# Optimization experiments

Measured on AMD Instinct MI355X. Metric: run time of the kernel, lower is better.

## Reference

```python
import jax, jax.numpy as jnp
import numpy as np

STATE_DIM = 5
HIDDEN = 32
B, S = 128, 4096
D_IN = STATE_DIM + 1 + 3  # [h_prev, temp_seq, direction]


def setup_inputs() -> dict:
    key = jax.random.key(0)
    ks = jax.random.split(key, 16)
    g = lambda k, shp: (jax.random.normal(k, shp, dtype=jnp.float32) * 0.1)
    z = lambda shp: jnp.zeros(shp, jnp.float32)
    inp = {}
    inp["h_prev"] = jax.random.normal(ks[0], (B, S, STATE_DIM), dtype=jnp.float32)
    inp["delta_x"] = jax.random.uniform(ks[1], (B, S, 6), dtype=jnp.float32)
    # internal layer 0 (input D_IN -> HIDDEN), layer 1 (HIDDEN -> HIDDEN)
    inp["Wa0"] = g(ks[2], (D_IN, HIDDEN)); inp["ba0"] = z((HIDDEN,))
    inp["Wb0"] = g(ks[3], (D_IN, HIDDEN)); inp["bb0"] = z((HIDDEN,))
    inp["Wa1"] = g(ks[4], (HIDDEN, HIDDEN)); inp["ba1"] = z((HIDDEN,))
    inp["Wb1"] = g(ks[5], (HIDDEN, HIDDEN)); inp["bb1"] = z((HIDDEN,))
    inp["W_alpha"] = g(ks[6], (HIDDEN, 1)); inp["b_alpha"] = z((1,))
    inp["W_beta"]  = g(ks[7], (HIDDEN, 1)); inp["b_beta"]  = z((1,))
    inp["W_gamma"] = g(ks[8], (HIDDEN, 1)); inp["b_gamma"] = z((1,))
    inp["W_c"] = g(ks[9], (HIDDEN, STATE_DIM)); inp["b_c"] = z((STATE_DIM,))
    inp["W_out"] = g(ks[10], (STATE_DIM, 1))  # no bias
    return inp


def reference(h_prev, delta_x, Wa0, ba0, Wb0, bb0, Wa1, ba1, Wb1, bb1,
              W_alpha, b_alpha, W_beta, b_beta, W_gamma, b_gamma,
              W_c, b_c, W_out):
    # delta_x: [delta_strain, delta_time, delta_temp, init_strain, init_time, init_temp]
    df = delta_x[..., :3]                       # (B, S, 3)
    init_temp = delta_x[:, 0:1, 5:6]            # (B, 1, 1) init temp at t=0
    temp_seq = jnp.cumsum(delta_x[..., 2:3], axis=1) + init_temp  # (B, S, 1)
    # normalized increment direction
    norm = jnp.maximum(jnp.sqrt(jnp.sum(df * df, axis=-1, keepdims=True)), 1e-7)
    direction = df / norm                       # (B, S, 3)
    l = jnp.concatenate([h_prev, temp_seq, direction], axis=-1)   # (B, S, 9)
    # two internal tanh*tanh gated dense layers
    l = jnp.tanh(l @ Wa0 + ba0) * jnp.tanh(l @ Wb0 + bb0)         # (B, S, 32)
    l = jnp.tanh(l @ Wa1 + ba1) * jnp.tanh(l @ Wb1 + bb1)         # (B, S, 32)
    # exp gates (non-negative rate params)
    alpha = jnp.exp(l @ W_alpha + b_alpha)      # (B, S, 1)
    beta  = jnp.exp(l @ W_beta  + b_beta)
    gamma = jnp.exp(l @ W_gamma + b_gamma)
    c_n = jnp.tanh(l @ W_c + b_c)               # (B, S, 5)
    # update gate from physical increments
    z = 1.0 - jnp.exp(-alpha * jnp.abs(df[..., 0:1])
                      - beta * df[..., 1:2]
                      - gamma * jnp.abs(df[..., 2:3]))
    h_n = (1.0 - z) * h_prev + z * c_n          # (B, S, 5)
    sigma_n = h_n @ W_out                       # (B, S, 1)
    return (h_n, sigma_n)
```

## Files before the change

kernel.cpp:

```cpp
#include <hip/hip_runtime.h>

#define B_DIMC   128
#define S_DIMC   4096
#define N_TOK    (B_DIMC * S_DIMC)
#define CHUNK    256
#define N_CHUNK  (N_TOK / CHUNK)
#define CPB      (S_DIMC / CHUNK)

typedef __attribute__((ext_vector_type(8))) short  short8;
typedef __attribute__((ext_vector_type(4))) float  floatx4;
typedef __attribute__((ext_vector_type(4))) int    intx4;

__device__ __forceinline__ int cvtpk(float a, float b) {
    int r;
    asm("v_cvt_pk_bf16_f32 %0, %1, %2" : "=v"(r) : "v"(a), "v"(b));
    return r;
}
__device__ __forceinline__ short bf1(float a) { return (short)cvtpk(a, a); }

__device__ __forceinline__ float fast_tanh(float x) {
    float e = __builtin_amdgcn_exp2f(2.885390082f * __builtin_amdgcn_fmed3f(x, -9.0f, 9.0f));
    return fmaf(-2.0f, __builtin_amdgcn_rcpf(e + 1.0f), 1.0f);
}
__device__ __forceinline__ float gate2(float a, float b) {
    const float c = 2.885390082f;
    float ea = __builtin_amdgcn_exp2f(c * __builtin_amdgcn_fmed3f(a, -9.0f, 9.0f));
    float eb = __builtin_amdgcn_exp2f(c * __builtin_amdgcn_fmed3f(b, -9.0f, 9.0f));
    float t  = fmaf(ea, eb, 1.0f);
    float u  = ea + eb;
    return (t - u) * __builtin_amdgcn_rcpf(t + u);
}

__device__ __forceinline__ float head_w(int n, int k,
                                        const float* Wal, const float* Wbe,
                                        const float* Wga, const float* Wc) {
    if (n == 0) return Wal[k];
    if (n == 1) return Wbe[k];
    if (n == 2) return Wga[k];
    if (n < 8)  return Wc[k * 5 + (n - 3)];
    return 0.0f;
}

union SMemU {
    struct {
        short W[4][32][40];
        short Wh[16][40];
        float Bias[16];
        float Wsum[4];
        float Wpre[4];
    } b;
    short A[4][64][40];
};

__global__ __launch_bounds__(256) void msc_kernel(
    const float* __restrict__ h_prev, const float* __restrict__ dx,
    const float* __restrict__ Wa0, const float* __restrict__ ba0,
    const float* __restrict__ Wb0, const float* __restrict__ bb0,
    const float* __restrict__ Wa1, const float* __restrict__ ba1,
    const float* __restrict__ Wb1, const float* __restrict__ bb1,
    const float* __restrict__ W_alpha, const float* __restrict__ b_alpha,
    const float* __restrict__ W_beta,  const float* __restrict__ b_beta,
    const float* __restrict__ W_gamma, const float* __restrict__ b_gamma,
    const float* __restrict__ W_c,     const float* __restrict__ b_c,
    const float* __restrict__ W_out,
    float* __restrict__ out)
{
    __shared__ __align__(16) SMemU sm;

    const int tid  = threadIdx.x;
    const int w    = tid >> 6;
    const int lane = tid & 63;
    const int n    = lane & 15;
    const int quad = lane >> 4;
    const int t    = blockIdx.x * CHUNK + tid;

    const float* hp = h_prev + (size_t)t * 5;
    const float* d  = dx     + (size_t)t * 6;
    const float hp0 = hp[0], hp1 = hp[1], hp2 = hp[2], hp3 = hp[3], hp4 = hp[4];
    const float df0 = d[0], df1 = d[1], df2 = d[2];

    const int batch = blockIdx.x / CPB;
    const int cib   = blockIdx.x % CPB;
    const float* dxb = dx + (size_t)batch * S_DIMC * 6;
    const int npre = cib * CHUNK;
    float ps = 0.0f;
    for (int s = tid; s < npre; s += 256)
        ps += dxb[(size_t)s * 6 + 2];
    ps += __shfl_xor(ps, 1, 64);
    ps += __shfl_xor(ps, 2, 64);
    ps += __shfl_xor(ps, 4, 64);
    ps += __shfl_xor(ps, 8, 64);
    ps += __shfl_xor(ps, 16, 64);
    ps += __shfl_xor(ps, 32, 64);
    if (lane == 0) sm.b.Wpre[w] = ps;

    float w5a[2], w5b[2], bA0[2], bB0[2], bA1[2], bB1[2];
    #pragma unroll
    for (int nt = 0; nt < 2; ++nt) {
        const int col = nt * 16 + n;
        w5a[nt] = Wa0[5 * 32 + col];  w5b[nt] = Wb0[5 * 32 + col];
        bA0[nt] = ba0[col];           bB0[nt] = bb0[col];
        bA1[nt] = ba1[col];           bB1[nt] = bb1[col];
    }

    float x = df2;
    #pragma unroll
    for (int off = 1; off < 64; off <<= 1) {
        float y = __shfl_up(x, off, 64);
        if (lane >= off) x += y;
    }
    if (lane == 63) sm.b.Wsum[w] = x;

    #pragma unroll
    for (int m = 0; m < 4; ++m) {
        const float* Wsrc = (m == 0) ? Wa0 : (m == 1) ? Wb0 : (m == 2) ? Wa1 : Wb1;
        const bool l0 = (m < 2);
        #pragma unroll
        for (int dd = tid; dd < 512; dd += 256) {
            const int col = dd >> 4, kd = dd & 15, k0 = kd * 2, k1 = k0 + 1;
            float v0, v1;
            if (l0) {
                v0 = (k0 < 9 && k0 != 5) ? Wsrc[k0 * 32 + col] : 0.0f;
                v1 = (k1 < 9 && k1 != 5) ? Wsrc[k1 * 32 + col] : 0.0f;
            } else {
                v0 = Wsrc[k0 * 32 + col];
                v1 = Wsrc[k1 * 32 + col];
            }
            ((int*)&sm.b.W[m][col][0])[kd] = cvtpk(v0, v1);
        }
    }
    {
        const int hn = tid >> 4, kd = tid & 15, k0 = kd * 2;
        const float v0 = head_w(hn, k0,     W_alpha, W_beta, W_gamma, W_c);
        const float v1 = head_w(hn, k0 + 1, W_alpha, W_beta, W_gamma, W_c);
        ((int*)&sm.b.Wh[hn][0])[kd] = cvtpk(v0, v1);
    }
    if (tid < 16) {
        sm.b.Bias[tid] = (tid == 0) ? b_alpha[0] : (tid == 1) ? b_beta[0]
                       : (tid == 2) ? b_gamma[0] : (tid < 8) ? b_c[tid - 3] : 0.0f;
    }

    __syncthreads();

    short8 Ba0f[2], Bb0f[2], Ba1f[2], Bb1f[2], Bhf;
    #pragma unroll
    for (int nt = 0; nt < 2; ++nt) {
        const int col = nt * 16 + n;
        Ba0f[nt] = *(const short8*)&sm.b.W[0][col][quad * 8];
        Bb0f[nt] = *(const short8*)&sm.b.W[1][col][quad * 8];
        Ba1f[nt] = *(const short8*)&sm.b.W[2][col][quad * 8];
        Bb1f[nt] = *(const short8*)&sm.b.W[3][col][quad * 8];
    }
    Bhf = *(const short8*)&sm.b.Wh[n][quad * 8];
    const float hbias = sm.b.Bias[n];

    const float coff = dxb[5]
        + (sm.b.Wpre[0] + sm.b.Wpre[1] + sm.b.Wpre[2] + sm.b.Wpre[3]);
    float pre = coff;
    if (w > 0) pre += sm.b.Wsum[0];
    if (w > 1) pre += sm.b.Wsum[1];
    if (w > 2) pre += sm.b.Wsum[2];
    const float temp_t = pre + x;

    __syncthreads();

    const float nrm = fmaxf(sqrtf(df0*df0 + df1*df1 + df2*df2), 1e-7f);
    const float inv = __builtin_amdgcn_rcpf(nrm);
    {
        int* arow = (int*)&sm.A[w][lane][0];
        intx4 v0 = { cvtpk(hp0, hp1), cvtpk(hp2, hp3),
                     cvtpk(hp4, 0.0f), cvtpk(df0*inv, df1*inv) };
        intx4 v1 = { cvtpk(df2*inv, 0.0f), 0, 0, 0 };
        intx4 z4 = { 0, 0, 0, 0 };
        *(intx4*)&arow[0]  = v0;
        *(intx4*)&arow[4]  = v1;
        *(intx4*)&arow[8]  = z4;
        *(intx4*)&arow[12] = z4;
        *(float*)&arow[16] = temp_t;
    }

    #pragma unroll
    for (int mt = 0; mt < 4; ++mt) {
        const short8 Af = *(const short8*)&sm.A[w][mt * 16 + n][quad * 8];
        const int rb = mt * 16 + quad * 4;
        floatx4 tv;
        #pragma unroll
        for (int r = 0; r < 4; ++r)
            tv[r] = *(const float*)&sm.A[w][rb + r][32];
        #pragma unroll
        for (int nt = 0; nt < 2; ++nt) {
            floatx4 Ca, Cb;
            #pragma unroll
            for (int r = 0; r < 4; ++r) {
                Ca[r] = fmaf(tv[r], w5a[nt], bA0[nt]);
                Cb[r] = fmaf(tv[r], w5b[nt], bB0[nt]);
            }
            Ca = __builtin_amdgcn_mfma_f32_16x16x32_bf16(Af, Ba0f[nt], Ca, 0, 0, 0);
            Cb = __builtin_amdgcn_mfma_f32_16x16x32_bf16(Af, Bb0f[nt], Cb, 0, 0, 0);
            #pragma unroll
            for (int r = 0; r < 4; ++r)
                sm.A[w][mt * 16 + quad * 4 + r][nt * 16 + n] = bf1(gate2(Ca[r], Cb[r]));
        }
    }

    #pragma unroll
    for (int mt = 0; mt < 4; ++mt) {
        const short8 Af = *(const short8*)&sm.A[w][mt * 16 + n][quad * 8];
        #pragma unroll
        for (int nt = 0; nt < 2; ++nt) {
            floatx4 Ca = { bA1[nt], bA1[nt], bA1[nt], bA1[nt] };
            floatx4 Cb = { bB1[nt], bB1[nt], bB1[nt], bB1[nt] };
            Ca = __builtin_amdgcn_mfma_f32_16x16x32_bf16(Af, Ba1f[nt], Ca, 0, 0, 0);
            Cb = __builtin_amdgcn_mfma_f32_16x16x32_bf16(Af, Bb1f[nt], Cb, 0, 0, 0);
            #pragma unroll
            for (int r = 0; r < 4; ++r)
                sm.A[w][mt * 16 + quad * 4 + r][nt * 16 + n] = bf1(gate2(Ca[r], Cb[r]));
        }
    }

    short8 Ah[4];
    #pragma unroll
    for (int mt = 0; mt < 4; ++mt)
        Ah[mt] = *(const short8*)&sm.A[w][mt * 16 + n][quad * 8];
    asm volatile("" ::: "memory");

    float* hc = (float*)&sm.A[w][0][0];
    #pragma unroll
    for (int mt = 0; mt < 4; ++mt) {
        floatx4 C = { hbias, hbias, hbias, hbias };
        C = __builtin_amdgcn_mfma_f32_16x16x32_bf16(Ah[mt], Bhf, C, 0, 0, 0);
        if (n < 8) {
            #pragma unroll
            for (int r = 0; r < 4; ++r)
                hc[(mt * 16 + quad * 4 + r) * 12 + n] = C[r];
        }
    }
    asm volatile("" ::: "memory");

    const floatx4 h0v = *(const floatx4*)&hc[lane * 12];
    const floatx4 h1v = *(const floatx4*)&hc[lane * 12 + 4];

    const float alpha = __expf(h0v[0]);
    const float beta  = __expf(h0v[1]);
    const float gamma = __expf(h0v[2]);
    const float z     = 1.0f - __expf(-(alpha * fabsf(df0) + beta * df1 + gamma * fabsf(df2)));
    const float omz   = 1.0f - z;

    const float c0 = fast_tanh(h0v[3]), c1 = fast_tanh(h1v[0]), c2 = fast_tanh(h1v[1]),
                c3 = fast_tanh(h1v[2]), c4 = fast_tanh(h1v[3]);

    const float hn0 = omz * hp0 + z * c0;
    const float hn1 = omz * hp1 + z * c1;
    const float hn2 = omz * hp2 + z * c2;
    const float hn3 = omz * hp3 + z * c3;
    const float hn4 = omz * hp4 + z * c4;

    float* out_h = out + (size_t)t * 5;
    out_h[0] = hn0; out_h[1] = hn1; out_h[2] = hn2; out_h[3] = hn3; out_h[4] = hn4;
    out[(size_t)N_TOK * 5 + t] =
        hn0 * W_out[0] + hn1 * W_out[1] + hn2 * W_out[2] + hn3 * W_out[3] + hn4 * W_out[4];
}

extern "C" void kernel_launch(void* const* d_in, const int* in_sizes, int n_in,
                              void* d_out, int out_size, void* d_ws, size_t ws_size,
                              hipStream_t stream) {
    const float* h_prev  = (const float*)d_in[0];
    const float* dx      = (const float*)d_in[1];
    const float* Wa0     = (const float*)d_in[2];
    const float* ba0     = (const float*)d_in[3];
    const float* Wb0     = (const float*)d_in[4];
    const float* bb0     = (const float*)d_in[5];
    const float* Wa1     = (const float*)d_in[6];
    const float* ba1     = (const float*)d_in[7];
    const float* Wb1     = (const float*)d_in[8];
    const float* bb1     = (const float*)d_in[9];
    const float* W_alpha = (const float*)d_in[10];
    const float* b_alpha = (const float*)d_in[11];
    const float* W_beta  = (const float*)d_in[12];
    const float* b_beta  = (const float*)d_in[13];
    const float* W_gamma = (const float*)d_in[14];
    const float* b_gamma = (const float*)d_in[15];
    const float* W_c     = (const float*)d_in[16];
    const float* b_c     = (const float*)d_in[17];
    const float* W_out   = (const float*)d_in[18];
    float* out = (float*)d_out;

    msc_kernel<<<N_CHUNK, CHUNK, 0, stream>>>(
        h_prev, dx,
        Wa0, ba0, Wb0, bb0, Wa1, ba1, Wb1, bb1,
        W_alpha, b_alpha, W_beta, b_beta, W_gamma, b_gamma,
        W_c, b_c, W_out, out);
}
```

Baseline: 140.2 us.

## Double chunk size to 512 tokens per block and vectorize prefix-sum reads

Blocks now cover 512 tokens with 8 waves, which halves the block count and shrinks the per-block redundant prefix scan over earlier chunks of the sequence. The prefix scan reads delta_x as float4 and keeps only the temperature-increment lanes by position modulo 3, so far fewer load instructions are issued. The weight-staging loop is simplified so each of the 512 threads writes one packed element per matrix. Larger blocks raise register and LDS demand per block and may lower occupancy. The code before has no visible indexing that assumes 4 waves beyond what was changed, though part of it is not shown.

```diff
diff --git a/kernel.cpp b/kernel.cpp
--- a/kernel.cpp
+++ b/kernel.cpp
@@ -3,7 +3,8 @@
 #define B_DIMC   128
 #define S_DIMC   4096
 #define N_TOK    (B_DIMC * S_DIMC)
-#define CHUNK    256
+#define CHUNK    512
+#define NWAVE    8
 #define N_CHUNK  (N_TOK / CHUNK)
 #define CPB      (S_DIMC / CHUNK)
 
@@ -46,13 +47,13 @@
         short W[4][32][40];
         short Wh[16][40];
         float Bias[16];
-        float Wsum[4];
-        float Wpre[4];
+        float Wsum[NWAVE];
+        float Wpre[NWAVE];
     } b;
-    short A[4][64][40];
+    short A[NWAVE][64][40];
 };
 
-__global__ __launch_bounds__(256) void msc_kernel(
+__global__ __launch_bounds__(512) void msc_kernel(
     const float* __restrict__ h_prev, const float* __restrict__ dx,
     const float* __restrict__ Wa0, const float* __restrict__ ba0,
     const float* __restrict__ Wb0, const float* __restrict__ bb0,
@@ -79,13 +80,17 @@
     const float hp0 = hp[0], hp1 = hp[1], hp2 = hp[2], hp3 = hp[3], hp4 = hp[4];
     const float df0 = d[0], df1 = d[1], df2 = d[2];
 
-    const int batch = blockIdx.x / CPB;
-    const int cib   = blockIdx.x % CPB;
+    const int batch = blockIdx.x >> 3;
+    const int cib   = blockIdx.x & 7;
     const float* dxb = dx + (size_t)batch * S_DIMC * 6;
-    const int npre = cib * CHUNK;
+    const int nf4 = cib * 768;
     float ps = 0.0f;
-    for (int s = tid; s < npre; s += 256)
-        ps += dxb[(size_t)s * 6 + 2];
+    for (int j = tid; j < nf4; j += 512) {
+        const float4 v = *(const float4*)(dxb + j * 4);
+        const int r = j % 3;
+        if (r == 0) ps += v.z;
+        if (r == 2) ps += v.x;
+    }
     ps += __shfl_xor(ps, 1, 64);
     ps += __shfl_xor(ps, 2, 64);
     ps += __shfl_xor(ps, 4, 64);
@@ -115,21 +120,18 @@
     for (int m = 0; m < 4; ++m) {
         const float* Wsrc = (m == 0) ? Wa0 : (m == 1) ? Wb0 : (m == 2) ? Wa1 : Wb1;
         const bool l0 = (m < 2);
-        #pragma unroll
-        for (int dd = tid; dd < 512; dd += 256) {
-            const int col = dd >> 4, kd = dd & 15, k0 = kd * 2, k1 = k0 + 1;
-            float v0, v1;
-            if (l0) {
-                v0 = (k0 < 9 && k0 != 5) ? Wsrc[k0 * 32 + col] : 0.0f;
-                v1 = (k1 < 9 && k1 != 5) ? Wsrc[k1 * 32 + col] : 0.0f;
-            } else {
-                v0 = Wsrc[k0 * 32 + col];
-                v1 = Wsrc[k1 * 32 + col];
-            }
-            ((int*)&sm.b.W[m][col][0])[kd] = cvtpk(v0, v1);
-        }
-    }
-    {
+        const int col = tid >> 4, kd = tid & 15, k0 = kd * 2, k1 = k0 + 1;
+        float v0, v1;
+        if (l0) {
+            v0 = (k0 < 9 && k0 != 5) ? Wsrc[k0 * 32 + col] : 0.0f;
+            v1 = (k1 < 9 && k1 != 5) ? Wsrc[k1 * 32 + col] : 0.0f;
+        } else {
+            v0 = Wsrc[k0 * 32 + col];
+            v1 = Wsrc[k1 * 32 + col];
+        }
+        ((int*)&sm.b.W[m][col][0])[kd] = cvtpk(v0, v1);
+    }
+    if (tid < 256) {
         const int hn = tid >> 4, kd = tid & 15, k0 = kd * 2;
         const float v0 = head_w(hn, k0,     W_alpha, W_beta, W_gamma, W_c);
         const float v1 = head_w(hn, k0 + 1, W_alpha, W_beta, W_gamma, W_c);
@@ -154,12 +156,12 @@
     Bhf = *(const short8*)&sm.b.Wh[n][quad * 8];
     const float hbias = sm.b.Bias[n];
 
-    const float coff = dxb[5]
-        + (sm.b.Wpre[0] + sm.b.Wpre[1] + sm.b.Wpre[2] + sm.b.Wpre[3]);
+    float coff = dxb[5];
+    #pragma unroll
+    for (int ww = 0; ww < NWAVE; ++ww) coff += sm.b.Wpre[ww];
     float pre = coff;
-    if (w > 0) pre += sm.b.Wsum[0];
-    if (w > 1) pre += sm.b.Wsum[1];
-    if (w > 2) pre += sm.b.Wsum[2];
+    #pragma unroll
+    for (int ww = 0; ww < NWAVE - 1; ++ww) if (w > ww) pre += sm.b.Wsum[ww];
     const float temp_t = pre + x;
 
     __syncthreads();
```

After: 136.0 us. 3.0% less time.
